# Performance work log

Hardware: AMD Instinct MI355X
Metric: run time of the kernel (lower is better)

The kernel has to match this reference:

```python
import jax, jax.numpy as jnp
import numpy as np


def _lstm_layer(x, W_ih, W_hh, b_ih, b_hh):
    # x: [B, T, D]; W_ih: [4H, D]; W_hh: [4H, H]; gate order (PyTorch): i, f, g, o
    B, T, _ = x.shape
    H = W_hh.shape[1]
    # Precompute input contributions for all timesteps: [B, T, 4H]
    xg = jnp.einsum('btd,gd->btg', x, W_ih) + b_ih + b_hh

    def step(carry, xg_t):
        h, c = carry
        gates = xg_t + h @ W_hh.T  # [B, 4H]
        i, f, g, o = jnp.split(gates, 4, axis=-1)
        i = jax.nn.sigmoid(i)
        f = jax.nn.sigmoid(f)
        g = jnp.tanh(g)
        o = jax.nn.sigmoid(o)
        c = f * c + i * g
        h = o * jnp.tanh(c)
        return (h, c), h

    h0 = jnp.zeros((B, H), dtype=x.dtype)
    c0 = jnp.zeros((B, H), dtype=x.dtype)
    (_, _), hs = jax.lax.scan(step, (h0, c0), jnp.swapaxes(xg, 0, 1))
    return jnp.swapaxes(hs, 0, 1)  # [B, T, H]


def setup_inputs() -> dict:
    key = jax.random.key(0)
    ks = jax.random.split(key, 11)
    B, T, D, H, C = 262144, 8, 8, 16, 10
    s = 1.0 / np.sqrt(H)  # PyTorch LSTM init scale
    return {
        'input_data': jax.random.normal(ks[0], (B, T, D), dtype=jnp.float32),
        'W_ih_l0': jax.random.uniform(ks[1], (4 * H, D), jnp.float32, -s, s),
        'W_hh_l0': jax.random.uniform(ks[2], (4 * H, H), jnp.float32, -s, s),
        'b_ih_l0': jax.random.uniform(ks[3], (4 * H,), jnp.float32, -s, s),
        'b_hh_l0': jax.random.uniform(ks[4], (4 * H,), jnp.float32, -s, s),
        'W_ih_l1': jax.random.uniform(ks[5], (4 * H, H), jnp.float32, -s, s),
        'W_hh_l1': jax.random.uniform(ks[6], (4 * H, H), jnp.float32, -s, s),
        'b_ih_l1': jax.random.uniform(ks[7], (4 * H,), jnp.float32, -s, s),
        'b_hh_l1': jax.random.uniform(ks[8], (4 * H,), jnp.float32, -s, s),
        'W_fc': jax.random.uniform(ks[9], (C, H), jnp.float32, -s, s),
        'b_fc': jax.random.uniform(ks[10], (C,), jnp.float32, -s, s),
    }


def reference(input_data, W_ih_l0, W_hh_l0, b_ih_l0, b_hh_l0,
              W_ih_l1, W_hh_l1, b_ih_l1, b_hh_l1, W_fc, b_fc):
    B = input_data.shape[0]
    x = input_data.reshape(B, 8, 8)
    h1 = _lstm_layer(x, W_ih_l0, W_hh_l0, b_ih_l0, b_hh_l0)   # [B, 8, 16]
    h2 = _lstm_layer(h1, W_ih_l1, W_hh_l1, b_ih_l1, b_hh_l1)  # [B, 8, 16]
    last = h2[:, -1, :]                                        # [B, 16]
    return last @ W_fc.T + b_fc                                # [B, 10]
```

## Files before the change

### kernel.cpp

```cpp
#include <hip/hip_runtime.h>

#define LOG2E 1.44269504088896340736f

typedef short    bf16x8 __attribute__((ext_vector_type(8)));
typedef _Float16 f16x8  __attribute__((ext_vector_type(8)));
typedef float    f32x4  __attribute__((ext_vector_type(4)));

template <int I> struct IntC { static constexpr int value = I; };
template <int I, int N, typename F>
__device__ __forceinline__ void sfor(F&& f) {
    if constexpr (I < N) { f(IntC<I>{}); sfor<I + 1, N>(f); }
}

__device__ __forceinline__ float fexp2(float x){ return __builtin_amdgcn_exp2f(x); }
__device__ __forceinline__ float frcp(float x){ return __builtin_amdgcn_rcpf(x); }

__device__ __forceinline__ float hi_part(float x){
    return __uint_as_float(__float_as_uint(x) & 0xFFFF0000u);
}
__device__ __forceinline__ unsigned pk2(float a, float b){
    return __builtin_amdgcn_perm(__float_as_uint(b), __float_as_uint(a), 0x07060302u);
}
__device__ __forceinline__ unsigned pk2lo(float a, float b){
    return pk2(a - hi_part(a), b - hi_part(b));
}
__device__ __forceinline__ unsigned pkh(float a, float b){
    unsigned short ua = __builtin_bit_cast(unsigned short, (_Float16)a);
    unsigned short ub = __builtin_bit_cast(unsigned short, (_Float16)b);
    return (unsigned)ua | ((unsigned)ub << 16);
}
__device__ __forceinline__ bf16x8 mkB(unsigned d0,unsigned d1,unsigned d2,unsigned d3){
    uint4 u{d0,d1,d2,d3};
    return __builtin_bit_cast(bf16x8, u);
}
__device__ __forceinline__ f16x8 mkBh(unsigned d0,unsigned d1,unsigned d2,unsigned d3){
    uint4 u{d0,d1,d2,d3};
    return __builtin_bit_cast(f16x8, u);
}

#define MFMA16  __builtin_amdgcn_mfma_f32_16x16x32_bf16
#define MFMA16H __builtin_amdgcn_mfma_f32_16x16x32_f16

__device__ __forceinline__ f32x4 cell_tail(const f32x4 (&dd)[4], f32x4& c){
    f32x4 Ei, Ef, Eg, Eo;
    sfor<0,4>([&](auto R){ constexpr int r=R.value;
        Ei[r] = fexp2(dd[0][r]);
        Ef[r] = fexp2(dd[1][r]);
        Eg[r] = fexp2(dd[2][r]);
        Eo[r] = fexp2(dd[3][r]);
    });
    f32x4 ov, cn;
    sfor<0,4>([&](auto R){ constexpr int r=R.value;
        float Ai = 1.f + Ei[r], Af = 1.f + Ef[r];
        float Ag = 1.f + Eg[r], Ao = 1.f + Eo[r];
        float p  = Ai*Af;  float rp = frcp(p);
        float iv = Af*rp;
        float fv = Ai*rp;
        float q2 = Ag*Ao;  float rq = frcp(q2);
        float gr = Ao*rq;
        ov[r]    = Ag*rq;
        float gv = (Eg[r]-1.f)*gr;
        cn[r] = fv*c[r] + iv*gv;
    });
    c = cn;
    f32x4 tc;
    sfor<0,4>([&](auto R){ constexpr int r=R.value;
        tc[r] = fexp2(cn[r]*(2.f*LOG2E));
    });
    float B0=tc[0]+1.f, B1=tc[1]+1.f, B2=tc[2]+1.f, B3=tc[3]+1.f;
    float P2=B0*B1, P3=P2*B2, P4=P3*B3;
    float r4=frcp(P4);
    float R3=P3*r4;
    float r3=B3*r4;
    float R2=P2*r3;
    float r2=B2*r3;
    float R1=B0*r2;
    float R0=B1*r2;
    f32x4 hv;
    hv[0] = ov[0]*((tc[0]-1.f)*R0);
    hv[1] = ov[1]*((tc[1]-1.f)*R1);
    hv[2] = ov[2]*((tc[2]-1.f)*R2);
    hv[3] = ov[3]*((tc[3]-1.f)*R3);
    return hv;
}

__global__
__attribute__((amdgpu_flat_work_group_size(256,256)))
__attribute__((amdgpu_waves_per_eu(1,8)))
void lstm_mfma_kernel(const float* __restrict__ in,
                      const float* __restrict__ Wih0, const float* __restrict__ Whh0,
                      const float* __restrict__ bih0, const float* __restrict__ bhh0,
                      const float* __restrict__ Wih1, const float* __restrict__ Whh1,
                      const float* __restrict__ bih1, const float* __restrict__ bhh1,
                      const float* __restrict__ Wfc,  const float* __restrict__ bfc,
                      float* __restrict__ out, int B)
{
    const int lane = threadIdx.x & 63;
    const int wid  = threadIdx.x >> 6;
    const int q  = lane >> 4;
    const int sl = lane & 15;
    const long s0 = (long)(blockIdx.x*4 + wid)*64;

    f16x8 a0[4], a1[4];
    f32x4 bias0[4], bias1[4];
    sfor<0,4>([&](auto MT){ constexpr int mt = MT.value;
        constexpr float SC = (mt==2) ? (2.f*LOG2E) : (-LOG2E);
        const int gr = 16*mt + sl;
        sfor<0,8>([&](auto E){ constexpr int e = E.value;
            float w0;
            if constexpr (e < 4)      w0 = Whh0[gr*16 + 4*q + e];
            else if constexpr (e < 6) w0 = Wih0[gr*8 + 2*q + (e-4)];
            else                      w0 = 0.f;
            a0[mt][e] = (_Float16)(w0 * SC);
            float w1;
            if constexpr (e < 4) w1 = Wih1[gr*16 + 4*q + e];
            else                 w1 = Whh1[gr*16 + 4*q + (e-4)];
            a1[mt][e] = (_Float16)(w1 * SC);
        });
        sfor<0,4>([&](auto R){ constexpr int r = R.value;
            const int gb = 16*mt + 4*q + r;
            bias0[mt][r] = (bih0[gb] + bhh0[gb]) * SC;
            bias1[mt][r] = (bih1[gb] + bhh1[gb]) * SC;
        });
    });

    unsigned P0h[4]={0,0,0,0}, Q0h[4]={0,0,0,0};
    unsigned P1h[4]={0,0,0,0}, Q1h[4]={0,0,0,0};
    f32x4 c0[4], c1[4], hl1[4];
    sfor<0,4>([&](auto G){ constexpr int g=G.value;
        c0[g] = f32x4{0,0,0,0}; c1[g] = f32x4{0,0,0,0};
        hl1[g] = f32x4{0,0,0,0};
    });

    const float* xbase = in + (s0 + sl)*64 + 2*q;
    float2 xv[4];
    sfor<0,4>([&](auto G){ constexpr int g=G.value;
        xv[g] = *(const float2*)(xbase + g*1024);
    });

#pragma unroll 2
    for (int t = 0; t < 8; ++t) {
        const int nxt = (t==7) ? 0 : (t+1)*8;
        float2 xn[4];
        sfor<0,4>([&](auto G){ constexpr int g=G.value;
            xn[g] = *(const float2*)(xbase + g*1024 + nxt);
        });

        sfor<0,4>([&](auto G){ constexpr int g=G.value;
            const unsigned xh = pkh(xv[g].x, xv[g].y);
            f16x8 Bh = mkBh(P0h[g], Q0h[g], xh, 0u);
            f32x4 dd[4];
            sfor<0,4>([&](auto MT){ constexpr int mt = MT.value;
                dd[mt] = MFMA16H(a0[mt], Bh, bias0[mt], 0,0,0);
            });
            f32x4 hv = cell_tail(dd, c0[g]);
            P0h[g] = pkh(hv[0],hv[1]);  Q0h[g] = pkh(hv[2],hv[3]);
        });

        sfor<0,4>([&](auto G){ constexpr int g=G.value;
            f16x8 Bh = mkBh(P0h[g], Q0h[g], P1h[g], Q1h[g]);
            f32x4 dd[4];
            sfor<0,4>([&](auto MT){ constexpr int mt = MT.value;
                dd[mt] = MFMA16H(a1[mt], Bh, bias1[mt], 0,0,0);
            });
            f32x4 hv = cell_tail(dd, c1[g]);
            hl1[g] = hv;
            P1h[g] = pkh(hv[0],hv[1]);  Q1h[g] = pkh(hv[2],hv[3]);
        });

        sfor<0,4>([&](auto G){ constexpr int g=G.value; xv[g] = xn[g]; });
    }

    {
        bf16x8 afh, afl;
        f32x4 biasf;
        sfor<0,8>([&](auto E){ constexpr int e = E.value;
            float wf = 0.f;
            if constexpr (e < 4) { if (sl < 10) wf = Wfc[sl*16 + 4*q + e]; }
            afh[e] = (short)(__float_as_uint(wf)>>16);
            afl[e] = (short)(__float_as_uint(wf - hi_part(wf))>>16);
        });
        sfor<0,4>([&](auto R){ constexpr int r = R.value;
            const int gb = 4*q + r;
            biasf[r] = (gb < 10) ? bfc[gb] : 0.f;
        });
        sfor<0,4>([&](auto G){ constexpr int g=G.value;
            const unsigned Fh0 = pk2(hl1[g][0], hl1[g][1]);
            const unsigned Fh1 = pk2(hl1[g][2], hl1[g][3]);
            const unsigned Fl0 = pk2lo(hl1[g][0], hl1[g][1]);
            const unsigned Fl1 = pk2lo(hl1[g][2], hl1[g][3]);
            bf16x8 Bh = mkB(Fh0, Fh1, 0u, 0u);
            bf16x8 Bl = mkB(Fl0, Fl1, 0u, 0u);
            f32x4 d = MFMA16(afl, Bh, biasf, 0,0,0);
            d = MFMA16(afh, Bl, d, 0,0,0);
            d = MFMA16(afh, Bh, d, 0,0,0);
            float* orow = out + (s0 + g*16 + sl)*10;
            if (q == 0)      { *(float2*)(orow+0) = float2{d[0],d[1]}; *(float2*)(orow+2) = float2{d[2],d[3]}; }
            else if (q == 1) { *(float2*)(orow+4) = float2{d[0],d[1]}; *(float2*)(orow+6) = float2{d[2],d[3]}; }
            else if (q == 2) { *(float2*)(orow+8) = float2{d[0],d[1]}; }
        });
    }
}

extern "C" void kernel_launch(void* const* d_in, const int* in_sizes, int n_in,
                              void* d_out, int out_size, void* d_ws, size_t ws_size,
                              hipStream_t stream) {
    const float* in   = (const float*)d_in[0];
    const float* Wih0 = (const float*)d_in[1];
    const float* Whh0 = (const float*)d_in[2];
    const float* bih0 = (const float*)d_in[3];
    const float* bhh0 = (const float*)d_in[4];
    const float* Wih1 = (const float*)d_in[5];
    const float* Whh1 = (const float*)d_in[6];
    const float* bih1 = (const float*)d_in[7];
    const float* bhh1 = (const float*)d_in[8];
    const float* Wfc  = (const float*)d_in[9];
    const float* bfc  = (const float*)d_in[10];
    float* out = (float*)d_out;

    int B = in_sizes[0] / 64;
    int grid = B / 256;
    lstm_mfma_kernel<<<grid, 256, 0, stream>>>(in, Wih0, Whh0, bih0, bhh0,
                                               Wih1, Whh1, bih1, bhh1,
                                               Wfc, bfc, out, B);
}
```

Before: 81.40 us.

## Use fp16 single-MFMA FC head, shared reciprocal in gates, pkrtz packing

The final FC layer swaps its three-pass split-bf16 MFMA for one fp16 MFMA that reuses the packed layer-1 hidden state, which removes the hl1 registers and the hi/lo splitting. The gate math now computes one reciprocal of the product of all four denominators instead of two, and f16 packing uses the cvt_pkrtz intrinsic. These cut instruction count and register pressure. In exchange the FC output precision drops to fp16, pkrtz rounds toward zero, and the product of four denominators can overflow for large exponents.

```diff
diff --git a/kernel.cpp b/kernel.cpp
--- a/kernel.cpp
+++ b/kernel.cpp
@@ -2,7 +2,6 @@
 
 #define LOG2E 1.44269504088896340736f
 
-typedef short    bf16x8 __attribute__((ext_vector_type(8)));
 typedef _Float16 f16x8  __attribute__((ext_vector_type(8)));
 typedef float    f32x4  __attribute__((ext_vector_type(4)));
 
@@ -15,30 +14,14 @@
 __device__ __forceinline__ float fexp2(float x){ return __builtin_amdgcn_exp2f(x); }
 __device__ __forceinline__ float frcp(float x){ return __builtin_amdgcn_rcpf(x); }
 
-__device__ __forceinline__ float hi_part(float x){
-    return __uint_as_float(__float_as_uint(x) & 0xFFFF0000u);
-}
-__device__ __forceinline__ unsigned pk2(float a, float b){
-    return __builtin_amdgcn_perm(__float_as_uint(b), __float_as_uint(a), 0x07060302u);
-}
-__device__ __forceinline__ unsigned pk2lo(float a, float b){
-    return pk2(a - hi_part(a), b - hi_part(b));
-}
 __device__ __forceinline__ unsigned pkh(float a, float b){
-    unsigned short ua = __builtin_bit_cast(unsigned short, (_Float16)a);
-    unsigned short ub = __builtin_bit_cast(unsigned short, (_Float16)b);
-    return (unsigned)ua | ((unsigned)ub << 16);
-}
-__device__ __forceinline__ bf16x8 mkB(unsigned d0,unsigned d1,unsigned d2,unsigned d3){
-    uint4 u{d0,d1,d2,d3};
-    return __builtin_bit_cast(bf16x8, u);
+    return __builtin_bit_cast(unsigned, __builtin_amdgcn_cvt_pkrtz(a, b));
 }
 __device__ __forceinline__ f16x8 mkBh(unsigned d0,unsigned d1,unsigned d2,unsigned d3){
     uint4 u{d0,d1,d2,d3};
     return __builtin_bit_cast(f16x8, u);
 }
 
-#define MFMA16  __builtin_amdgcn_mfma_f32_16x16x32_bf16
 #define MFMA16H __builtin_amdgcn_mfma_f32_16x16x32_f16
 
 __device__ __forceinline__ f32x4 cell_tail(const f32x4 (&dd)[4], f32x4& c){
@@ -53,12 +36,13 @@
     sfor<0,4>([&](auto R){ constexpr int r=R.value;
         float Ai = 1.f + Ei[r], Af = 1.f + Ef[r];
         float Ag = 1.f + Eg[r], Ao = 1.f + Eo[r];
-        float p  = Ai*Af;  float rp = frcp(p);
-        float iv = Af*rp;
-        float fv = Ai*rp;
-        float q2 = Ag*Ao;  float rq = frcp(q2);
-        float gr = Ao*rq;
-        ov[r]    = Ag*rq;
+        float L2 = Ai*Af, L3 = L2*Ag, P4 = L3*Ao;
+        float S2 = Ag*Ao, S1 = Af*S2;
+        float r4 = frcp(P4);
+        float iv = S1*r4;
+        float fv = (Ai*S2)*r4;
+        float gr = (L2*Ao)*r4;
+        ov[r]    = L3*r4;
         float gv = (Eg[r]-1.f)*gr;
         cn[r] = fv*c[r] + iv*gv;
     });
@@ -126,10 +110,9 @@
 
     unsigned P0h[4]={0,0,0,0}, Q0h[4]={0,0,0,0};
     unsigned P1h[4]={0,0,0,0}, Q1h[4]={0,0,0,0};
-    f32x4 c0[4], c1[4], hl1[4];
+    f32x4 c0[4], c1[4];
     sfor<0,4>([&](auto G){ constexpr int g=G.value;
         c0[g] = f32x4{0,0,0,0}; c1[g] = f32x4{0,0,0,0};
-        hl1[g] = f32x4{0,0,0,0};
     });
 
     const float* xbase = in + (s0 + sl)*64 + 2*q;
@@ -164,7 +147,6 @@
                 dd[mt] = MFMA16H(a1[mt], Bh, bias1[mt], 0,0,0);
             });
             f32x4 hv = cell_tail(dd, c1[g]);
-            hl1[g] = hv;
             P1h[g] = pkh(hv[0],hv[1]);  Q1h[g] = pkh(hv[2],hv[3]);
         });
 
@@ -172,28 +154,20 @@
     }
 
     {
-        bf16x8 afh, afl;
+        f16x8 af;
         f32x4 biasf;
         sfor<0,8>([&](auto E){ constexpr int e = E.value;
             float wf = 0.f;
             if constexpr (e < 4) { if (sl < 10) wf = Wfc[sl*16 + 4*q + e]; }
-            afh[e] = (short)(__float_as_uint(wf)>>16);
-            afl[e] = (short)(__float_as_uint(wf - hi_part(wf))>>16);
+            af[e] = (_Float16)wf;
         });
         sfor<0,4>([&](auto R){ constexpr int r = R.value;
             const int gb = 4*q + r;
             biasf[r] = (gb < 10) ? bfc[gb] : 0.f;
         });
         sfor<0,4>([&](auto G){ constexpr int g=G.value;
-            const unsigned Fh0 = pk2(hl1[g][0], hl1[g][1]);
-            const unsigned Fh1 = pk2(hl1[g][2], hl1[g][3]);
-            const unsigned Fl0 = pk2lo(hl1[g][0], hl1[g][1]);
-            const unsigned Fl1 = pk2lo(hl1[g][2], hl1[g][3]);
-            bf16x8 Bh = mkB(Fh0, Fh1, 0u, 0u);
-            bf16x8 Bl = mkB(Fl0, Fl1, 0u, 0u);
-            f32x4 d = MFMA16(afl, Bh, biasf, 0,0,0);
-            d = MFMA16(afh, Bl, d, 0,0,0);
-            d = MFMA16(afh, Bh, d, 0,0,0);
+            f16x8 Bh = mkBh(P1h[g], Q1h[g], 0u, 0u);
+            f32x4 d = MFMA16H(af, Bh, biasf, 0,0,0);
             float* orow = out + (s0 + g*16 + sl)*10;
             if (q == 0)      { *(float2*)(orow+0) = float2{d[0],d[1]}; *(float2*)(orow+2) = float2{d[2],d[3]}; }
             else if (q == 1) { *(float2*)(orow+4) = float2{d[0],d[1]}; *(float2*)(orow+6) = float2{d[2],d[3]}; }
```

Result: slower. 89.04 us (+9.4%).
